# Kernel tuning notes

Measured on AMD Instinct MI355X. Metric: run time of the kernel, lower is better.

## Reference

```python
import jax, jax.numpy as jnp
import numpy as np

H = 4            # heads
C = 64           # per-head dim (= hidden, PyG TransformerConv semantics)
HD = 64          # hidden_dim
L = 2            # num_layers
NT = 2           # node types: 0=task, 1=machine
ET = ((0, 1), (1, 0))  # edge types: (src_nt, dst_nt)
N = 16384        # nodes per type (== max_nodes -> simple pos-enc slice)
E = 262144       # edges per edge type


def _ln(x, g, b):
    mu = x.mean(-1, keepdims=True)
    var = ((x - mu) ** 2).mean(-1, keepdims=True)
    return (x - mu) * jax.lax.rsqrt(var + 1e-5) * g + b


def _tconv(x_src, x_dst, ei, Wq, bq, Wk, bk, Wv, bv, Ws, bs, Wb):
    # PyG TransformerConv: heads=H, out_channels=C, concat=False, beta=True
    n_dst = x_dst.shape[0]
    src, dst = ei[0], ei[1]
    q = (x_dst @ Wq + bq).reshape(-1, H, C)
    k = (x_src @ Wk + bk).reshape(-1, H, C)
    v = (x_src @ Wv + bv).reshape(-1, H, C)
    logits = jnp.einsum('ehc,ehc->eh', q[dst], k[src]) * (1.0 / float(np.sqrt(C)))  # [E,H]
    m = jax.ops.segment_max(logits, dst, num_segments=n_dst)          # [N,H] segment softmax
    ex = jnp.exp(logits - m[dst])
    denom = jax.ops.segment_sum(ex, dst, num_segments=n_dst)
    alpha = ex / denom[dst]                                            # [E,H]
    msg = (alpha[:, :, None] * v[src]).reshape(-1, H * C)              # [E,H*C]
    out = jax.ops.segment_sum(msg, dst, num_segments=n_dst)
    out = out.reshape(n_dst, H, C).mean(axis=1)                        # concat=False -> head mean
    r = x_dst @ Ws + bs                                                # lin_skip
    beta = jax.nn.sigmoid(jnp.concatenate([out, r, out - r], -1) @ Wb) # lin_beta, [N,1]
    return beta * r + (1.0 - beta) * out


def _forward(edge_index, x, W_in, b_in, type_emb, pos, Wq, bq, Wk, bk, Wv, bv,
             Wskip, bskip, Wbeta, ln_g, ln_b, ff_W1, ff_b1, ff_W2, ff_b2, W_out, b_out):
    # input proj + type embedding + positional encoding (num_nodes == max_nodes -> slice)
    h = [x[t] @ W_in[t] + b_in[t] + type_emb[t] + pos[t] for t in range(NT)]
    for l in range(L):
        hn = [jnp.zeros_like(h[0]), jnp.zeros_like(h[1])]
        for e, (s, d) in enumerate(ET):  # HeteroConv, aggr='sum'
            hn[d] = hn[d] + _tconv(h[s], h[d], edge_index[e],
                                   Wq[l, e], bq[l, e], Wk[l, e], bk[l, e],
                                   Wv[l, e], bv[l, e], Wskip[l, e], bskip[l, e], Wbeta[l, e])
        for t in range(NT):
            hr = _ln(h[t] + hn[t], ln_g[l, t], ln_b[l, t])
            ff = jax.nn.gelu(hr @ ff_W1[l, t] + ff_b1[l, t], approximate=False) @ ff_W2[l, t] + ff_b2[l, t]
            h[t] = hr + ff
    return jnp.stack([h[t] @ W_out[t] + b_out[t] for t in range(NT)])  # [NT,N,HD]


def setup_inputs() -> dict:
    key = jax.random.key(0)
    ks = jax.random.split(key, 16)
    w = lambda k, s: 0.02 * jax.random.normal(k, s, jnp.float32)
    NE = len(ET)
    return {
        'x': jax.random.normal(ks[0], (NT, N, HD), jnp.float32),
        'edge_index': jax.random.randint(ks[1], (NE, 2, E), 0, N, jnp.int32),
        'W_in': w(ks[2], (NT, HD, HD)), 'b_in': jnp.zeros((NT, HD), jnp.float32),
        'type_emb': w(ks[3], (NT, HD)),
        'pos': w(ks[4], (NT, N, HD)),
        'Wq': w(ks[5], (L, NE, HD, H * C)), 'bq': jnp.zeros((L, NE, H * C), jnp.float32),
        'Wk': w(ks[6], (L, NE, HD, H * C)), 'bk': jnp.zeros((L, NE, H * C), jnp.float32),
        'Wv': w(ks[7], (L, NE, HD, H * C)), 'bv': jnp.zeros((L, NE, H * C), jnp.float32),
        'Wskip': w(ks[8], (L, NE, HD, HD)), 'bskip': jnp.zeros((L, NE, HD), jnp.float32),
        'Wbeta': w(ks[9], (L, NE, 3 * HD, 1)),
        'ln_g': jnp.ones((L, NT, HD), jnp.float32), 'ln_b': jnp.zeros((L, NT, HD), jnp.float32),
        'ff_W1': w(ks[10], (L, NT, HD, 4 * HD)), 'ff_b1': jnp.zeros((L, NT, 4 * HD), jnp.float32),
        'ff_W2': w(ks[11], (L, NT, 4 * HD, HD)), 'ff_b2': jnp.zeros((L, NT, HD), jnp.float32),
        'W_out': w(ks[12], (NT, HD, HD)), 'b_out': jnp.zeros((NT, HD), jnp.float32),
    }


def reference(x, edge_index, W_in, b_in, type_emb, pos, Wq, bq, Wk, bk, Wv, bv,
              Wskip, bskip, Wbeta, ln_g, ln_b, ff_W1, ff_b1, ff_W2, ff_b2, W_out, b_out):
    return _forward(edge_index, x, W_in, b_in, type_emb, pos, Wq, bq, Wk, bk, Wv, bv,
                    Wskip, bskip, Wbeta, ln_g, ln_b, ff_W1, ff_b1, ff_W2, ff_b2, W_out, b_out)
```

## Files before the change

kernel.cpp:

```cpp
#include <hip/hip_runtime.h>
#include <math.h>

#define NN 16384
#define EE 262144

typedef __bf16 v8bf __attribute__((ext_vector_type(8)));
typedef __bf16 v4bf __attribute__((ext_vector_type(4)));
typedef float  v4f  __attribute__((ext_vector_type(4)));
typedef float  v2f  __attribute__((ext_vector_type(2)));

#define OFF_CNT     0
#define OFF_FILL    (2*NN)
#define OFF_ROWPTR  (4*NN)
#define OFF_COLSRC  98816
#define OFF_H       623104
#define OFF_HN      (OFF_H  + 2*NN*64)
#define OFF_Q       (OFF_HN + 2*NN*64)
#define OFF_KV      (OFF_Q  + 2*NN*128)
#define OFF_R       (OFF_KV + 2*NN*128)
#define OFF_WT      (OFF_R  + 2*NN*64)
#define OFF_WBP     (OFF_WT + 180224)
#define OFF_LNG     (OFF_WBP + 768)
#define OFF_LNB     (OFF_LNG + 256)


#define WT_Q   0
#define WT_K   65536
#define WT_V   131072
#define WT_S   196608
#define WT_IN  212992
#define WT_W1  221184
#define WT_W2  286720
#define WT_WO  352256

__device__ __forceinline__ float blo(unsigned u) { return __uint_as_float(u << 16); }
__device__ __forceinline__ float bhi(unsigned u) { return __uint_as_float(u & 0xffff0000u); }
__device__ __forceinline__ unsigned short f2b(float f) {
  __bf16 h = (__bf16)f;
  return *(unsigned short*)&h;
}

struct PrepDesc { const float* src; unsigned short* dst; int ksh; int total; int kperm; };
struct PrepPack { PrepDesc d[28]; };

__global__ __launch_bounds__(256) void prep_kernel(PrepPack p) {
  PrepDesc g = p.d[blockIdx.y];
  int idx = blockIdx.x * 256 + threadIdx.x;
  if (idx >= g.total) return;
  int K = 1 << g.ksh;
  int n = idx >> g.ksh;
  int k = idx & (K - 1);
  int N = g.total >> g.ksh;
  int kk = g.kperm ? (16 * (k & 3) + (k >> 2)) : k;
  g.dst[idx] = f2b(g.src[(size_t)kk * N + n]);
}

struct PermDesc { const float* src; float* dst; int total; };
struct PermPack { PermDesc d[3]; };

__global__ __launch_bounds__(256) void perm_kernel(PermPack p) {
  PermDesc g = p.d[blockIdx.y];
  int idx = blockIdx.x * 256 + threadIdx.x;
  if (idx >= g.total) return;
  int c = idx & 63;
  g.dst[(idx & ~63) + ((c & 15) << 2) + (c >> 4)] = g.src[idx];
}

__global__ void count_kernel(const int* __restrict__ ei, int* __restrict__ cnt) {
  int idx = blockIdx.x * 256 + threadIdx.x;
  if (idx >= 2 * EE) return;
  int et = idx >> 18;
  int j  = idx & (EE - 1);
  int dst = ei[et * 2 * EE + EE + j];
  atomicAdd(&cnt[et * NN + dst], 1);
}

__global__ __launch_bounds__(1024) void scan_kernel(const int* __restrict__ cnt,
                                                    int* __restrict__ rowptr,
                                                    int* __restrict__ fill) {
  int et = blockIdx.x;
  const int* c = cnt + et * NN;
  __shared__ int sums[1024];
  int tid = threadIdx.x;
  int base = tid * 16;
  int loc[16];
  int s = 0;
#pragma unroll
  for (int i = 0; i < 16; ++i) { loc[i] = s; s += c[base + i]; }
  sums[tid] = s;
  __syncthreads();
  for (int off = 1; off < 1024; off <<= 1) {
    int v = 0;
    if (tid >= off) v = sums[tid - off];
    __syncthreads();
    if (tid >= off) sums[tid] += v;
    __syncthreads();
  }
  int ebase = (tid == 0) ? 0 : sums[tid - 1];
  int* rp = rowptr + et * (NN + 1);
  int* fl = fill + et * NN;
#pragma unroll
  for (int i = 0; i < 16; ++i) {
    rp[base + i] = ebase + loc[i];
    fl[base + i] = ebase + loc[i];
  }
  if (tid == 1023) rp[NN] = sums[1023];
}

__global__ void scatter_kernel(const int* __restrict__ ei, int* __restrict__ fill,
                               int* __restrict__ colsrc) {
  int idx = blockIdx.x * 256 + threadIdx.x;
  if (idx >= 2 * EE) return;
  int et = idx >> 18;
  int j  = idx & (EE - 1);
  int src = ei[et * 2 * EE + j];
  int dst = ei[et * 2 * EE + EE + j];
  int pos = atomicAdd(&fill[et * NN + dst], 1);
  colsrc[et * EE + pos] = (et * NN + src) << 9;
}

struct GemmDesc {
  const float *A, *bias, *bias2, *add;
  const unsigned short* Bt;
  char* C;
  int Ncols, Cld, ntiles, gelu, otype;
};
struct GemmPack { GemmDesc d[8]; int nd; };

#define LDA 72

__global__ __launch_bounds__(256) void gemm_mfma(GemmPack p) {
  GemmDesc g = p.d[blockIdx.y];
  const int row0 = blockIdx.x * 128;
  const int tid = threadIdx.x;
  const int w = tid >> 6, lane = tid & 63;
  const int l16 = lane & 15, quad = lane >> 4;

  __shared__ __bf16 As[128 * LDA];
  __shared__ __bf16 Bs[64 * LDA];

#pragma unroll
  for (int it = 0; it < 8; ++it) {
    int fi = it * 256 + tid;
    int grow = fi >> 4;
    int kq = (fi & 15) << 2;
    float4 a = *(const float4*)(g.A + (size_t)(row0 + grow) * 64 + kq);
    v4bf c = { (__bf16)a.x, (__bf16)a.y, (__bf16)a.z, (__bf16)a.w };
    *(v4bf*)&As[grow * LDA + kq] = c;
  }

  const int brow = tid >> 2;
  const int bko  = (tid & 3) << 4;

  for (int ct0 = 0; ct0 < g.ntiles; ++ct0) {
    const int col0 = ct0 * 64;
    __syncthreads();
    {
      const unsigned short* bp = g.Bt + (size_t)(col0 + brow) * 64 + bko;
      uint4 b0 = *(const uint4*)(bp);
      uint4 b1 = *(const uint4*)(bp + 8);
      *(uint4*)&Bs[brow * LDA + bko] = b0;
      *(uint4*)&Bs[brow * LDA + bko + 8] = b1;
    }
    __syncthreads();

    v4f acc[2][4];
#pragma unroll
    for (int rt = 0; rt < 2; ++rt)
#pragma unroll
      for (int ct = 0; ct < 4; ++ct)
#pragma unroll
        for (int r = 0; r < 4; ++r) acc[rt][ct][r] = 0.f;

#pragma unroll
    for (int ks = 0; ks < 2; ++ks) {
      v8bf a0 = *(v8bf*)&As[(w * 32 + l16) * LDA + ks * 32 + quad * 8];
      v8bf a1 = *(v8bf*)&As[(w * 32 + 16 + l16) * LDA + ks * 32 + quad * 8];
#pragma unroll
      for (int ct = 0; ct < 4; ++ct) {
        v8bf bb = *(v8bf*)&Bs[(ct * 16 + l16) * LDA + ks * 32 + quad * 8];
        acc[0][ct] = __builtin_amdgcn_mfma_f32_16x16x32_bf16(a0, bb, acc[0][ct], 0, 0, 0);
        acc[1][ct] = __builtin_amdgcn_mfma_f32_16x16x32_bf16(a1, bb, acc[1][ct], 0, 0, 0);
      }
    }

    float bias_c[4];
#pragma unroll
    for (int ct = 0; ct < 4; ++ct) {
      int col = col0 + ct * 16 + l16;
      float b = g.bias ? g.bias[col] : 0.f;
      if (g.bias2) b += g.bias2[col];
      bias_c[ct] = b;
    }
#pragma unroll
    for (int rt = 0; rt < 2; ++rt)
#pragma unroll
      for (int r = 0; r < 4; ++r) {
        size_t row = row0 + w * 32 + rt * 16 + quad * 4 + r;
        char* cp = g.C + row * (size_t)g.Cld;
        if (g.otype == 0) {
          float vv[4];
#pragma unroll
          for (int ct = 0; ct < 4; ++ct) {
            int col = col0 + ct * 16 + l16;
            float v = acc[rt][ct][r] + bias_c[ct];
            if (g.add) v += g.add[row * g.Ncols + col];
            if (g.gelu) v = 0.5f * v * (1.f + erff(v * 0.70710678118654752f));
            vv[ct] = v;
          }
          float4 w4 = { vv[0], vv[1], vv[2], vv[3] };
          *(float4*)(cp + col0 * 4 + l16 * 16) = w4;
        } else if (g.otype == 1) {
          ushort4 wq;
          wq.x = f2b(acc[rt][0][r] + bias_c[0]);
          wq.y = f2b(acc[rt][1][r] + bias_c[1]);
          wq.z = f2b(acc[rt][2][r] + bias_c[2]);
          wq.w = f2b(acc[rt][3][r] + bias_c[3]);
          *(ushort4*)(cp + col0 * 2 + l16 * 8) = wq;
        } else {
          unsigned wv = 0;
#pragma unroll
          for (int ct = 0; ct < 4; ++ct) {
            float v = acc[rt][ct][r] + bias_c[ct];
            unsigned pk = __builtin_amdgcn_cvt_pk_fp8_f32(v, v, 0, false);
            wv |= (pk & 0xffu) << (8 * ct);
          }
          *(unsigned*)(cp + col0 + l16 * 4) = wv;
        }
      }
  }
}

struct FFPack {
  const float *HN;
  const unsigned short *W1t, *W2t, *Wot;
  const float *b1, *b2, *bout;
  float* H;
  float* outbuf;
};

__global__ __launch_bounds__(256) void ff_fused(FFPack p) {
  const int t = blockIdx.y;
  const int row0 = blockIdx.x * 64;
  const int tid = threadIdx.x;
  const int w = tid >> 6, lane = tid & 63;
  const int l16 = lane & 15, quad = lane >> 4;

  const float* A  = p.HN + ((size_t)t * NN) * 64;
  const unsigned short* W1t = p.W1t + (size_t)t * 16384;
  const unsigned short* W2t = p.W2t + (size_t)t * 16384;
  const float* b1 = p.b1 + t * 256;
  const float* b2 = p.b2 + t * 64;

  __shared__ __bf16 As[64 * LDA];
  __shared__ __bf16 A2[64 * LDA];
  __shared__ __bf16 B1s[64 * LDA];
  __shared__ __bf16 B2s[64 * LDA];

#pragma unroll
  for (int it = 0; it < 4; ++it) {
    int fi = it * 256 + tid;
    int grow = fi >> 4;
    int kq = (fi & 15) << 2;
    float4 a = *(const float4*)(A + (size_t)(row0 + grow) * 64 + kq);
    v4bf c = { (__bf16)a.x, (__bf16)a.y, (__bf16)a.z, (__bf16)a.w };
    *(v4bf*)&As[grow * LDA + kq] = c;
  }

  const int brow = tid >> 2;
  const int bko  = (tid & 3) << 4;

  v4f acc2[4];
#pragma unroll
  for (int ct = 0; ct < 4; ++ct)
#pragma unroll
    for (int r = 0; r < 4; ++r) acc2[ct][r] = 0.f;

  for (int c1 = 0; c1 < 4; ++c1) {
    {
      const unsigned short* bp1 = W1t + (size_t)(c1 * 64 + brow) * 64 + bko;
      uint4 u0 = *(const uint4*)(bp1);
      uint4 u1 = *(const uint4*)(bp1 + 8);
      *(uint4*)&B1s[brow * LDA + bko] = u0;
      *(uint4*)&B1s[brow * LDA + bko + 8] = u1;
      const unsigned short* bp2 = W2t + (size_t)brow * 256 + c1 * 64 + bko;
      uint4 u2 = *(const uint4*)(bp2);
      uint4 u3 = *(const uint4*)(bp2 + 8);
      *(uint4*)&B2s[brow * LDA + bko] = u2;
      *(uint4*)&B2s[brow * LDA + bko + 8] = u3;
    }
    __syncthreads();

    v4f acc1[4];
#pragma unroll
    for (int ct = 0; ct < 4; ++ct)
#pragma unroll
      for (int r = 0; r < 4; ++r) acc1[ct][r] = 0.f;
#pragma unroll
    for (int ks = 0; ks < 2; ++ks) {
      v8bf a = *(v8bf*)&As[(w * 16 + l16) * LDA + ks * 32 + quad * 8];
#pragma unroll
      for (int ct = 0; ct < 4; ++ct) {
        v8bf bb = *(v8bf*)&B1s[(ct * 16 + l16) * LDA + ks * 32 + quad * 8];
        acc1[ct] = __builtin_amdgcn_mfma_f32_16x16x32_bf16(a, bb, acc1[ct], 0, 0, 0);
      }
    }
#pragma unroll
    for (int ct = 0; ct < 4; ++ct) {
      float bb = b1[c1 * 64 + ct * 16 + l16];
#pragma unroll
      for (int r = 0; r < 4; ++r) {
        float v = acc1[ct][r] + bb;
        v = 0.5f * v * (1.f + erff(v * 0.70710678118654752f));
        A2[(w * 16 + quad * 4 + r) * LDA + ct * 16 + l16] = (__bf16)v;
      }
    }
#pragma unroll
    for (int ks = 0; ks < 2; ++ks) {
      v8bf a = *(v8bf*)&A2[(w * 16 + l16) * LDA + ks * 32 + quad * 8];
#pragma unroll
      for (int ct = 0; ct < 4; ++ct) {
        v8bf bb = *(v8bf*)&B2s[(ct * 16 + l16) * LDA + ks * 32 + quad * 8];
        acc2[ct] = __builtin_amdgcn_mfma_f32_16x16x32_bf16(a, bb, acc2[ct], 0, 0, 0);
      }
    }
    __syncthreads();
  }

  float b2c[4];
#pragma unroll
  for (int ct = 0; ct < 4; ++ct) b2c[ct] = b2[ct * 16 + l16];

  if (!p.outbuf) {
#pragma unroll
    for (int r = 0; r < 4; ++r) {
      size_t row = (size_t)t * NN + row0 + w * 16 + quad * 4 + r;
      float4 hn4 = *(const float4*)(p.HN + row * 64 + l16 * 4);
      float4 o4;
      o4.x = acc2[0][r] + b2c[0] + hn4.x;
      o4.y = acc2[1][r] + b2c[1] + hn4.y;
      o4.z = acc2[2][r] + b2c[2] + hn4.z;
      o4.w = acc2[3][r] + b2c[3] + hn4.w;
      *(float4*)(p.H + row * 64 + l16 * 4) = o4;
    }
    return;
  }

#pragma unroll
  for (int r = 0; r < 4; ++r) {
    int lrow = w * 16 + quad * 4 + r;
    size_t row = (size_t)t * NN + row0 + lrow;
    float4 hn4 = *(const float4*)(p.HN + row * 64 + l16 * 4);
    float hn[4] = { hn4.x, hn4.y, hn4.z, hn4.w };
#pragma unroll
    for (int ct = 0; ct < 4; ++ct) {
      int col = ct * 16 + l16;
      A2[lrow * LDA + col] = (__bf16)(acc2[ct][r] + b2c[ct] + hn[ct]);
    }
  }
  {
    const unsigned short* Wot = p.Wot + (size_t)t * 4096;
    const unsigned short* bp = Wot + (size_t)brow * 64 + bko;
    uint4 u0 = *(const uint4*)(bp);
    uint4 u1 = *(const uint4*)(bp + 8);
    *(uint4*)&B1s[brow * LDA + bko] = u0;
    *(uint4*)&B1s[brow * LDA + bko + 8] = u1;
  }
  __syncthreads();

  v4f acc3[4];
#pragma unroll
  for (int ct = 0; ct < 4; ++ct)
#pragma unroll
    for (int r = 0; r < 4; ++r) acc3[ct][r] = 0.f;
#pragma unroll
  for (int ks = 0; ks < 2; ++ks) {
    v8bf a = *(v8bf*)&A2[(w * 16 + l16) * LDA + ks * 32 + quad * 8];
#pragma unroll
    for (int ct = 0; ct < 4; ++ct) {
      v8bf bb = *(v8bf*)&B1s[(ct * 16 + l16) * LDA + ks * 32 + quad * 8];
      acc3[ct] = __builtin_amdgcn_mfma_f32_16x16x32_bf16(a, bb, acc3[ct], 0, 0, 0);
    }
  }
  const float* bo = p.bout + t * 64;
#pragma unroll
  for (int ct = 0; ct < 4; ++ct) {
    int col = ct * 16 + l16;
    float bb = bo[col];
#pragma unroll
    for (int r = 0; r < 4; ++r) {
      size_t row = (size_t)t * NN + row0 + w * 16 + quad * 4 + r;
      p.outbuf[row * 64 + col] = acc3[ct][r] + bb;
    }
  }
}

struct AggPack {
  const unsigned short *Q;
  const char *KV;
  const float *R;
  const float *Wb;
  const float *Hin;
  const float *lng, *lnb;
  float* outHR;
  const int *rowptr;
  const int *colsrc;
};

__global__ __launch_bounds__(256) void agg_kernel(AggPack p) {
  const int et = blockIdx.y, d = 1 - et;
  int wid = __builtin_amdgcn_readfirstlane(threadIdx.x >> 6);
  int lane = threadIdx.x & 63;
  int node = blockIdx.x * 4 + wid;
  int c4 = lane & 15;
  int cb = ((lane >> 4) << 6) + (c4 << 2);

  const int* rp = p.rowptr + et * (NN + 1);
  const int* cs = p.colsrc + et * EE;
  int start = rp[node], end = rp[node + 1];
  int len = end - start;
  int gnode = d * NN + node;

  uint2 qw = *(const uint2*)(p.Q + ((size_t)gnode << 8) + cb);
  float q0 = blo(qw.x) * 0.125f, q1 = bhi(qw.x) * 0.125f;
  float q2 = blo(qw.y) * 0.125f, q3 = bhi(qw.y) * 0.125f;

  int b[5];
#pragma unroll
  for (int i = 0; i <= 4; ++i) b[i] = start + ((len * i) >> 2);
  float dsum[4] = {0.f, 0.f, 0.f, 0.f};
  float acc[4][4];
#pragma unroll
  for (int s4 = 0; s4 < 4; ++s4)
#pragma unroll
    for (int c = 0; c < 4; ++c) acc[s4][c] = 0.f;

  int maxn = (len + 3) >> 2;
  int last = end - 1;
  for (int it = 0; it < maxn; ++it) {
#pragma unroll
    for (int s4 = 0; s4 < 4; ++s4) {
      int j = b[s4] + it;
      bool act = j < b[s4 + 1];
      int jc = act ? j : last;
      int off = cs[jc];
      const char* rowp = p.KV + off;
      unsigned kw = *(const unsigned*)(rowp + cb);
      unsigned vw = *(const unsigned*)(rowp + 256 + cb);
      v2f kl = __builtin_amdgcn_cvt_pk_f32_fp8((int)kw, false);
      v2f kh = __builtin_amdgcn_cvt_pk_f32_fp8((int)kw, true);
      float pd = q0 * kl[0] + q1 * kl[1] + q2 * kh[0] + q3 * kh[1];
      pd += __shfl_xor(pd, 1);
      pd += __shfl_xor(pd, 2);
      pd += __shfl_xor(pd, 4);
      pd += __shfl_xor(pd, 8);
      float wgt = act ? __expf(pd) : 0.f;
      v2f vl = __builtin_amdgcn_cvt_pk_f32_fp8((int)vw, false);
      v2f vh = __builtin_amdgcn_cvt_pk_f32_fp8((int)vw, true);
      dsum[s4] += wgt;
      acc[s4][0] += wgt * vl[0];
      acc[s4][1] += wgt * vl[1];
      acc[s4][2] += wgt * vh[0];
      acc[s4][3] += wgt * vh[1];
    }
  }
  float dn = (dsum[0] + dsum[1]) + (dsum[2] + dsum[3]);
  float o_[4];
#pragma unroll
  for (int i = 0; i < 4; ++i)
    o_[i] = (acc[0][i] + acc[1][i]) + (acc[2][i] + acc[3][i]);

  float inv = (len > 0) ? (0.25f / dn) : 0.f;
#pragma unroll
  for (int i = 0; i < 4; ++i) {
    float a = o_[i] * inv;
    a += __shfl_xor(a, 16);
    a += __shfl_xor(a, 32);
    o_[i] = a;
  }

  float4 r4 = *(const float4*)(p.R + (size_t)gnode * 64 + c4 * 4);
  float4 h4 = *(const float4*)(p.Hin + (size_t)gnode * 64 + c4 * 4);
  float rr[4] = { r4.x, r4.y, r4.z, r4.w };
  float hh[4] = { h4.x, h4.y, h4.z, h4.w };

  const float* wb = p.Wb + et * 192;
  float4 wo4 = *(const float4*)(wb + c4 * 4);
  float4 wr4 = *(const float4*)(wb + 64 + c4 * 4);
  float4 wd4 = *(const float4*)(wb + 128 + c4 * 4);
  float wo[4] = { wo4.x, wo4.y, wo4.z, wo4.w };
  float wr[4] = { wr4.x, wr4.y, wr4.z, wr4.w };
  float wd[4] = { wd4.x, wd4.y, wd4.z, wd4.w };
  float part = 0.f;
#pragma unroll
  for (int i = 0; i < 4; ++i)
    part += o_[i] * wo[i] + rr[i] * wr[i] + (o_[i] - rr[i]) * wd[i];
  part += __shfl_xor(part, 1);
  part += __shfl_xor(part, 2);
  part += __shfl_xor(part, 4);
  part += __shfl_xor(part, 8);
  float beta = 1.f / (1.f + __expf(-part));

  float y[4];
  float sa = 0.f, sb = 0.f;
#pragma unroll
  for (int i = 0; i < 4; ++i) {
    float v = hh[i] + beta * rr[i] + (1.f - beta) * o_[i];
    y[i] = v;
    sa += v;
    sb += v * v;
  }
  sa += __shfl_xor(sa, 1); sb += __shfl_xor(sb, 1);
  sa += __shfl_xor(sa, 2); sb += __shfl_xor(sb, 2);
  sa += __shfl_xor(sa, 4); sb += __shfl_xor(sb, 4);
  sa += __shfl_xor(sa, 8); sb += __shfl_xor(sb, 8);
  float mu = sa * (1.f / 64.f);
  float var = sb * (1.f / 64.f) - mu * mu;
  float rs = rsqrtf(var + 1e-5f);
  if (lane < 16) {
    float4 g4 = *(const float4*)(p.lng + d * 64 + c4 * 4);
    float4 bb4 = *(const float4*)(p.lnb + d * 64 + c4 * 4);
    float4 res;
    res.x = (y[0] - mu) * rs * g4.x + bb4.x;
    res.y = (y[1] - mu) * rs * g4.y + bb4.y;
    res.z = (y[2] - mu) * rs * g4.z + bb4.z;
    res.w = (y[3] - mu) * rs * g4.w + bb4.w;
    *(float4*)(p.outHR + (size_t)gnode * 64 + c4 * 4) = res;
  }
}

static void add_desc(GemmPack& p, const float* A, const unsigned short* Bt,
                     const float* bias, const float* bias2, const float* add,
                     void* C, int Nc, int Cld, int gelu, int otype) {
  GemmDesc& g = p.d[p.nd++];
  g.A = A; g.Bt = Bt; g.bias = bias; g.bias2 = bias2; g.add = add; g.C = (char*)C;
  g.Ncols = Nc; g.Cld = Cld; g.ntiles = Nc / 64;
  g.gelu = gelu; g.otype = otype;
}

extern "C" void kernel_launch(void* const* d_in, const int* in_sizes, int n_in,
                              void* d_out, int out_size, void* d_ws, size_t ws_size,
                              hipStream_t stream) {
  const float* x        = (const float*)d_in[0];
  const int*   ei       = (const int*)d_in[1];
  const float* W_in     = (const float*)d_in[2];
  const float* b_in     = (const float*)d_in[3];
  const float* type_emb = (const float*)d_in[4];
  const float* pos      = (const float*)d_in[5];
  const float* Wq       = (const float*)d_in[6];
  const float* bq       = (const float*)d_in[7];
  const float* Wk       = (const float*)d_in[8];
  const float* bk       = (const float*)d_in[9];
  const float* Wv       = (const float*)d_in[10];
  const float* bv       = (const float*)d_in[11];
  const float* Wskip    = (const float*)d_in[12];
  const float* bskip    = (const float*)d_in[13];
  const float* Wbeta    = (const float*)d_in[14];
  const float* ln_g     = (const float*)d_in[15];
  const float* ln_b     = (const float*)d_in[16];
  const float* ff_W1    = (const float*)d_in[17];
  const float* ff_b1    = (const float*)d_in[18];
  const float* ff_W2    = (const float*)d_in[19];
  const float* ff_b2    = (const float*)d_in[20];
  const float* W_out    = (const float*)d_in[21];
  const float* b_out    = (const float*)d_in[22];
  float* out = (float*)d_out;

  int*   wsi = (int*)d_ws;
  float* wsf = (float*)d_ws;
  int* cnt    = wsi + OFF_CNT;
  int* fill   = wsi + OFF_FILL;
  int* rowptr = wsi + OFF_ROWPTR;
  int* colsrc = wsi + OFF_COLSRC;
  float* H  = wsf + OFF_H;
  float* HN = wsf + OFF_HN;
  unsigned short* Qb = (unsigned short*)(wsf + OFF_Q);
  char* KVb = (char*)(wsf + OFF_KV);
  float* Rb = wsf + OFF_R;
  unsigned short* wt = (unsigned short*)(wsf + OFF_WT);
  float* wbp  = wsf + OFF_WBP;
  float* lngp = wsf + OFF_LNG;
  float* lnbp = wsf + OFF_LNB;

  {
    PrepPack pp{};
    int nd = 0;
    for (int we = 0; we < 4; ++we) {
      pp.d[nd++] = { Wq + (size_t)we * 16384, wt + WT_Q + we * 16384, 6, 16384, 1 };
      pp.d[nd++] = { Wk + (size_t)we * 16384, wt + WT_K + we * 16384, 6, 16384, 1 };
      pp.d[nd++] = { Wv + (size_t)we * 16384, wt + WT_V + we * 16384, 6, 16384, 1 };
      pp.d[nd++] = { Wskip + (size_t)we * 4096, wt + WT_S + we * 4096, 6, 4096, 1 };
      pp.d[nd++] = { ff_W1 + (size_t)we * 16384, wt + WT_W1 + we * 16384, 6, 16384, 1 };
      pp.d[nd++] = { ff_W2 + (size_t)we * 16384, wt + WT_W2 + we * 16384, 8, 16384, 0 };
    }
    for (int t = 0; t < 2; ++t) {
      pp.d[nd++] = { W_in + (size_t)t * 4096, wt + WT_IN + t * 4096, 6, 4096, 0 };
      pp.d[nd++] = { W_out + (size_t)t * 4096, wt + WT_WO + t * 4096, 6, 4096, 0 };
    }
    prep_kernel<<<dim3(64, nd), dim3(256), 0, stream>>>(pp);
  }
  {
    PermPack pm{};
    pm.d[0] = { Wbeta, wbp, 768 };
    pm.d[1] = { ln_g, lngp, 256 };
    pm.d[2] = { ln_b, lnbp, 256 };
    perm_kernel<<<dim3(3, 3), dim3(256), 0, stream>>>(pm);
  }

  hipMemsetAsync(cnt, 0, 2 * NN * sizeof(int), stream);
  count_kernel<<<dim3(2 * EE / 256), dim3(256), 0, stream>>>(ei, cnt);
  scan_kernel<<<dim3(2), dim3(1024), 0, stream>>>(cnt, rowptr, fill);
  scatter_kernel<<<dim3(2 * EE / 256), dim3(256), 0, stream>>>(ei, fill, colsrc);

  {
    GemmPack p{};
    for (int t = 0; t < 2; ++t)
      add_desc(p, x + (size_t)t * NN * 64, wt + WT_IN + t * 4096,
               b_in + t * 64, type_emb + t * 64, pos + (size_t)t * NN * 64,
               H + (size_t)t * NN * 64, 64, 256, 0, 0);
    gemm_mfma<<<dim3(128, p.nd), dim3(256), 0, stream>>>(p);
  }

  for (int l = 0; l < 2; ++l) {
    {
      GemmPack p{};
      for (int et = 0; et < 2; ++et) {
        int s = et, d = 1 - et;
        int we = l * 2 + et;
        const float* hs = H + (size_t)s * NN * 64;
        const float* hd = H + (size_t)d * NN * 64;
        add_desc(p, hd, wt + WT_Q + we * 16384, bq + we * 256,
                 nullptr, nullptr, (char*)Qb + (size_t)d * NN * 512, 256, 512, 0, 1);
        add_desc(p, hs, wt + WT_K + we * 16384, bk + we * 256,
                 nullptr, nullptr, KVb + (size_t)s * NN * 512, 256, 512, 0, 2);
        add_desc(p, hs, wt + WT_V + we * 16384, bv + we * 256,
                 nullptr, nullptr, KVb + (size_t)s * NN * 512 + 256, 256, 512, 0, 2);
        add_desc(p, hd, wt + WT_S + we * 4096, bskip + we * 64,
                 nullptr, nullptr, Rb + (size_t)d * NN * 64, 64, 256, 0, 0);
      }
      gemm_mfma<<<dim3(128, p.nd), dim3(256), 0, stream>>>(p);
    }

    AggPack ap;
    ap.Q = Qb; ap.KV = KVb; ap.R = Rb;
    ap.Wb = wbp + l * 2 * 192;
    ap.Hin = H;
    ap.lng = lngp + l * 128;
    ap.lnb = lnbp + l * 128;
    ap.outHR = HN;
    ap.rowptr = rowptr;
    ap.colsrc = colsrc;
    agg_kernel<<<dim3(NN / 4, 2), dim3(256), 0, stream>>>(ap);

    FFPack fp;
    fp.HN = HN;
    fp.W1t = wt + WT_W1 + l * 2 * 16384;
    fp.W2t = wt + WT_W2 + l * 2 * 16384;
    fp.Wot = wt + WT_WO;
    fp.b1 = ff_b1 + l * 2 * 256;
    fp.b2 = ff_b2 + l * 2 * 64;
    fp.bout = b_out;
    fp.H  = H;
    fp.outbuf = (l == 1) ? out : nullptr;
    ff_fused<<<dim3(NN / 64, 2), dim3(256), 0, stream>>>(fp);
  }
}
```

Measured before the change: 321.7 us.

## Fuse next-layer QKV/skip projections into FF epilogue and merge prep launches

The layer-0 feed-forward kernel now keeps its output tile in shared memory as bf16 and computes the layer-1 Q, K, V and skip projections directly in a 13-tile loop. This removes the separate layer-1 projection GEMM launch and the re-read of H from global memory. The perm kernel and the count memset are folded into the prep kernel as extra modes. The count and scatter kernels now process four edges per thread using int4 loads. The fused FF kernel does more serial work per block, adding per-tile syncs and register pressure that may reduce overlap.

```diff
diff --git a/kernel.cpp b/kernel.cpp
--- a/kernel.cpp
+++ b/kernel.cpp
@@ -40,39 +40,36 @@
   return *(unsigned short*)&h;
 }
 
-struct PrepDesc { const float* src; unsigned short* dst; int ksh; int total; int kperm; };
-struct PrepPack { PrepDesc d[28]; };
+struct PrepDesc { const float* src; void* dst; int ksh; int total; int mode; };
+struct PrepPack { PrepDesc d[34]; };
 
 __global__ __launch_bounds__(256) void prep_kernel(PrepPack p) {
   PrepDesc g = p.d[blockIdx.y];
   int idx = blockIdx.x * 256 + threadIdx.x;
   if (idx >= g.total) return;
+  if (g.mode == 3) { ((int*)g.dst)[idx] = 0; return; }
+  if (g.mode == 2) {
+    int c = idx & 63;
+    ((float*)g.dst)[(idx & ~63) + ((c & 15) << 2) + (c >> 4)] = g.src[idx];
+    return;
+  }
   int K = 1 << g.ksh;
   int n = idx >> g.ksh;
   int k = idx & (K - 1);
   int N = g.total >> g.ksh;
-  int kk = g.kperm ? (16 * (k & 3) + (k >> 2)) : k;
-  g.dst[idx] = f2b(g.src[(size_t)kk * N + n]);
-}
-
-struct PermDesc { const float* src; float* dst; int total; };
-struct PermPack { PermDesc d[3]; };
-
-__global__ __launch_bounds__(256) void perm_kernel(PermPack p) {
-  PermDesc g = p.d[blockIdx.y];
-  int idx = blockIdx.x * 256 + threadIdx.x;
-  if (idx >= g.total) return;
-  int c = idx & 63;
-  g.dst[(idx & ~63) + ((c & 15) << 2) + (c >> 4)] = g.src[idx];
+  int kk = (g.mode == 1) ? (16 * (k & 3) + (k >> 2)) : k;
+  ((unsigned short*)g.dst)[idx] = f2b(g.src[(size_t)kk * N + n]);
 }
 
 __global__ void count_kernel(const int* __restrict__ ei, int* __restrict__ cnt) {
   int idx = blockIdx.x * 256 + threadIdx.x;
-  if (idx >= 2 * EE) return;
-  int et = idx >> 18;
-  int j  = idx & (EE - 1);
-  int dst = ei[et * 2 * EE + EE + j];
-  atomicAdd(&cnt[et * NN + dst], 1);
+  int et = idx >> 16;
+  int j4 = (idx & 65535) << 2;
+  int4 dv = *(const int4*)(ei + (size_t)et * 2 * EE + EE + j4);
+  atomicAdd(&cnt[et * NN + dv.x], 1);
+  atomicAdd(&cnt[et * NN + dv.y], 1);
+  atomicAdd(&cnt[et * NN + dv.z], 1);
+  atomicAdd(&cnt[et * NN + dv.w], 1);
 }
 
 __global__ __launch_bounds__(1024) void scan_kernel(const int* __restrict__ cnt,
@@ -110,13 +107,18 @@
 __global__ void scatter_kernel(const int* __restrict__ ei, int* __restrict__ fill,
                                int* __restrict__ colsrc) {
   int idx = blockIdx.x * 256 + threadIdx.x;
-  if (idx >= 2 * EE) return;
-  int et = idx >> 18;
-  int j  = idx & (EE - 1);
-  int src = ei[et * 2 * EE + j];
-  int dst = ei[et * 2 * EE + EE + j];
-  int pos = atomicAdd(&fill[et * NN + dst], 1);
-  colsrc[et * EE + pos] = (et * NN + src) << 9;
+  int et = idx >> 16;
+  int j4 = (idx & 65535) << 2;
+  const int* eb = ei + (size_t)et * 2 * EE;
+  int4 sv = *(const int4*)(eb + j4);
+  int4 dv = *(const int4*)(eb + EE + j4);
+  int* fl = fill + et * NN;
+  int* csb = colsrc + et * EE;
+  int pos;
+  pos = atomicAdd(&fl[dv.x], 1); csb[pos] = (et * NN + sv.x) << 9;
+  pos = atomicAdd(&fl[dv.y], 1); csb[pos] = (et * NN + sv.y) << 9;
+  pos = atomicAdd(&fl[dv.z], 1); csb[pos] = (et * NN + sv.z) << 9;
+  pos = atomicAdd(&fl[dv.w], 1); csb[pos] = (et * NN + sv.w) << 9;
 }
 
 struct GemmDesc {
@@ -231,12 +233,16 @@
   }
 }
 
+struct QTile { const unsigned short* Bt; const float* bias; char* C; int Cld; int otype; };
+
 struct FFPack {
   const float *HN;
   const unsigned short *W1t, *W2t, *Wot;
   const float *b1, *b2, *bout;
   float* H;
   float* outbuf;
+  QTile qt[2][13];
+  int nqt;
 };
 
 __global__ __launch_bounds__(256) void ff_fused(FFPack p) {
@@ -331,17 +337,53 @@
 #pragma unroll
   for (int ct = 0; ct < 4; ++ct) b2c[ct] = b2[ct * 16 + l16];
 
-  if (!p.outbuf) {
+  if (p.outbuf) {
 #pragma unroll
     for (int r = 0; r < 4; ++r) {
-      size_t row = (size_t)t * NN + row0 + w * 16 + quad * 4 + r;
+      int lrow = w * 16 + quad * 4 + r;
+      size_t row = (size_t)t * NN + row0 + lrow;
       float4 hn4 = *(const float4*)(p.HN + row * 64 + l16 * 4);
-      float4 o4;
-      o4.x = acc2[0][r] + b2c[0] + hn4.x;
-      o4.y = acc2[1][r] + b2c[1] + hn4.y;
-      o4.z = acc2[2][r] + b2c[2] + hn4.z;
-      o4.w = acc2[3][r] + b2c[3] + hn4.w;
-      *(float4*)(p.H + row * 64 + l16 * 4) = o4;
+      float hn[4] = { hn4.x, hn4.y, hn4.z, hn4.w };
+#pragma unroll
+      for (int ct = 0; ct < 4; ++ct) {
+        int col = ct * 16 + l16;
+        A2[lrow * LDA + col] = (__bf16)(acc2[ct][r] + b2c[ct] + hn[ct]);
+      }
+    }
+    {
+      const unsigned short* Wot = p.Wot + (size_t)t * 4096;
+      const unsigned short* bp = Wot + (size_t)brow * 64 + bko;
+      uint4 u0 = *(const uint4*)(bp);
+      uint4 u1 = *(const uint4*)(bp + 8);
+      *(uint4*)&B1s[brow * LDA + bko] = u0;
+      *(uint4*)&B1s[brow * LDA + bko + 8] = u1;
+    }
+    __syncthreads();
+
+    v4f acc3[4];
+#pragma unroll
+    for (int ct = 0; ct < 4; ++ct)
+#pragma unroll
+      for (int r = 0; r < 4; ++r) acc3[ct][r] = 0.f;
+#pragma unroll
+    for (int ks = 0; ks < 2; ++ks) {
+      v8bf a = *(v8bf*)&A2[(w * 16 + l16) * LDA + ks * 32 + quad * 8];
+#pragma unroll
+      for (int ct = 0; ct < 4; ++ct) {
+        v8bf bb = *(v8bf*)&B1s[(ct * 16 + l16) * LDA + ks * 32 + quad * 8];
+        acc3[ct] = __builtin_amdgcn_mfma_f32_16x16x32_bf16(a, bb, acc3[ct], 0, 0, 0);
+      }
+    }
+    const float* bo = p.bout + t * 64;
+#pragma unroll
+    for (int ct = 0; ct < 4; ++ct) {
+      int col = ct * 16 + l16;
+      float bb = bo[col];
+#pragma unroll
+      for (int r = 0; r < 4; ++r) {
+        size_t row = (size_t)t * NN + row0 + w * 16 + quad * 4 + r;
+        p.outbuf[row * 64 + col] = acc3[ct][r] + bb;
+      }
     }
     return;
   }
@@ -351,46 +393,72 @@
     int lrow = w * 16 + quad * 4 + r;
     size_t row = (size_t)t * NN + row0 + lrow;
     float4 hn4 = *(const float4*)(p.HN + row * 64 + l16 * 4);
-    float hn[4] = { hn4.x, hn4.y, hn4.z, hn4.w };
-#pragma unroll
-    for (int ct = 0; ct < 4; ++ct) {
-      int col = ct * 16 + l16;
-      A2[lrow * LDA + col] = (__bf16)(acc2[ct][r] + b2c[ct] + hn[ct]);
-    }
-  }
-  {
-    const unsigned short* Wot = p.Wot + (size_t)t * 4096;
-    const unsigned short* bp = Wot + (size_t)brow * 64 + bko;
-    uint4 u0 = *(const uint4*)(bp);
-    uint4 u1 = *(const uint4*)(bp + 8);
-    *(uint4*)&B1s[brow * LDA + bko] = u0;
-    *(uint4*)&B1s[brow * LDA + bko + 8] = u1;
-  }
-  __syncthreads();
-
-  v4f acc3[4];
-#pragma unroll
-  for (int ct = 0; ct < 4; ++ct)
-#pragma unroll
-    for (int r = 0; r < 4; ++r) acc3[ct][r] = 0.f;
-#pragma unroll
-  for (int ks = 0; ks < 2; ++ks) {
-    v8bf a = *(v8bf*)&A2[(w * 16 + l16) * LDA + ks * 32 + quad * 8];
-#pragma unroll
-    for (int ct = 0; ct < 4; ++ct) {
-      v8bf bb = *(v8bf*)&B1s[(ct * 16 + l16) * LDA + ks * 32 + quad * 8];
-      acc3[ct] = __builtin_amdgcn_mfma_f32_16x16x32_bf16(a, bb, acc3[ct], 0, 0, 0);
-    }
-  }
-  const float* bo = p.bout + t * 64;
-#pragma unroll
-  for (int ct = 0; ct < 4; ++ct) {
-    int col = ct * 16 + l16;
-    float bb = bo[col];
+    float4 o4;
+    o4.x = acc2[0][r] + b2c[0] + hn4.x;
+    o4.y = acc2[1][r] + b2c[1] + hn4.y;
+    o4.z = acc2[2][r] + b2c[2] + hn4.z;
+    o4.w = acc2[3][r] + b2c[3] + hn4.w;
+    *(float4*)(p.H + row * 64 + l16 * 4) = o4;
+    v4bf a4 = { (__bf16)o4.x, (__bf16)o4.y, (__bf16)o4.z, (__bf16)o4.w };
+    *(v4bf*)&As[lrow * LDA + l16 * 4] = a4;
+  }
+
+  for (int ti = 0; ti < p.nqt; ++ti) {
+    QTile qt = p.qt[t][ti];
+    __syncthreads();
+    {
+      const unsigned short* bp = qt.Bt + (size_t)brow * 64 + bko;
+      uint4 u0 = *(const uint4*)(bp);
+      uint4 u1 = *(const uint4*)(bp + 8);
+      *(uint4*)&B1s[brow * LDA + bko] = u0;
+      *(uint4*)&B1s[brow * LDA + bko + 8] = u1;
+    }
+    __syncthreads();
+
+    v4f acc1[4];
+#pragma unroll
+    for (int ct = 0; ct < 4; ++ct)
+#pragma unroll
+      for (int r = 0; r < 4; ++r) acc1[ct][r] = 0.f;
+#pragma unroll
+    for (int ks = 0; ks < 2; ++ks) {
+      v8bf a = *(v8bf*)&As[(w * 16 + l16) * LDA + ks * 32 + quad * 8];
+#pragma unroll
+      for (int ct = 0; ct < 4; ++ct) {
+        v8bf bb = *(v8bf*)&B1s[(ct * 16 + l16) * LDA + ks * 32 + quad * 8];
+        acc1[ct] = __builtin_amdgcn_mfma_f32_16x16x32_bf16(a, bb, acc1[ct], 0, 0, 0);
+      }
+    }
+
+    float bias_c[4];
+#pragma unroll
+    for (int ct = 0; ct < 4; ++ct) bias_c[ct] = qt.bias[ct * 16 + l16];
+
 #pragma unroll
     for (int r = 0; r < 4; ++r) {
-      size_t row = (size_t)t * NN + row0 + w * 16 + quad * 4 + r;
-      p.outbuf[row * 64 + col] = acc3[ct][r] + bb;
+      size_t row = row0 + w * 16 + quad * 4 + r;
+      char* cp = qt.C + row * (size_t)qt.Cld;
+      if (qt.otype == 0) {
+        float4 w4 = { acc1[0][r] + bias_c[0], acc1[1][r] + bias_c[1],
+                      acc1[2][r] + bias_c[2], acc1[3][r] + bias_c[3] };
+        *(float4*)(cp + l16 * 16) = w4;
+      } else if (qt.otype == 1) {
+        ushort4 wq;
+        wq.x = f2b(acc1[0][r] + bias_c[0]);
+        wq.y = f2b(acc1[1][r] + bias_c[1]);
+        wq.z = f2b(acc1[2][r] + bias_c[2]);
+        wq.w = f2b(acc1[3][r] + bias_c[3]);
+        *(ushort4*)(cp + l16 * 8) = wq;
+      } else {
+        unsigned wv = 0;
+#pragma unroll
+        for (int ct = 0; ct < 4; ++ct) {
+          float v = acc1[ct][r] + bias_c[ct];
+          unsigned pk = __builtin_amdgcn_cvt_pk_fp8_f32(v, v, 0, false);
+          wv |= (pk & 0xffu) << (8 * ct);
+        }
+        *(unsigned*)(cp + l16 * 4) = wv;
+      }
     }
   }
 }
@@ -597,20 +665,17 @@
       pp.d[nd++] = { W_in + (size_t)t * 4096, wt + WT_IN + t * 4096, 6, 4096, 0 };
       pp.d[nd++] = { W_out + (size_t)t * 4096, wt + WT_WO + t * 4096, 6, 4096, 0 };
     }
+    pp.d[nd++] = { Wbeta, wbp, 0, 768, 2 };
+    pp.d[nd++] = { ln_g, lngp, 0, 256, 2 };
+    pp.d[nd++] = { ln_b, lnbp, 0, 256, 2 };
+    pp.d[nd++] = { nullptr, cnt, 0, 16384, 3 };
+    pp.d[nd++] = { nullptr, cnt + 16384, 0, 16384, 3 };
     prep_kernel<<<dim3(64, nd), dim3(256), 0, stream>>>(pp);
   }
-  {
-    PermPack pm{};
-    pm.d[0] = { Wbeta, wbp, 768 };
-    pm.d[1] = { ln_g, lngp, 256 };
-    pm.d[2] = { ln_b, lnbp, 256 };
-    perm_kernel<<<dim3(3, 3), dim3(256), 0, stream>>>(pm);
-  }
-
-  hipMemsetAsync(cnt, 0, 2 * NN * sizeof(int), stream);
-  count_kernel<<<dim3(2 * EE / 256), dim3(256), 0, stream>>>(ei, cnt);
+
+  count_kernel<<<dim3(2 * EE / 1024), dim3(256), 0, stream>>>(ei, cnt);
   scan_kernel<<<dim3(2), dim3(1024), 0, stream>>>(cnt, rowptr, fill);
-  scatter_kernel<<<dim3(2 * EE / 256), dim3(256), 0, stream>>>(ei, fill, colsrc);
+  scatter_kernel<<<dim3(2 * EE / 1024), dim3(256), 0, stream>>>(ei, fill, colsrc);
 
   {
     GemmPack p{};
@@ -621,26 +686,26 @@
     gemm_mfma<<<dim3(128, p.nd), dim3(256), 0, stream>>>(p);
   }
 
+  {
+    GemmPack p{};
+    for (int et = 0; et < 2; ++et) {
+      int s = et, d = 1 - et;
+      int we = et;
+      const float* hs = H + (size_t)s * NN * 64;
+      const float* hd = H + (size_t)d * NN * 64;
+      add_desc(p, hd, wt + WT_Q + we * 16384, bq + we * 256,
+               nullptr, nullptr, (char*)Qb + (size_t)d * NN * 512, 256, 512, 0, 1);
+      add_desc(p, hs, wt + WT_K + we * 16384, bk + we * 256,
+               nullptr, nullptr, KVb + (size_t)s * NN * 512, 256, 512, 0, 2);
+      add_desc(p, hs, wt + WT_V + we * 16384, bv + we * 256,
+               nullptr, nullptr, KVb + (size_t)s * NN * 512 + 256, 256, 512, 0, 2);
+      add_desc(p, hd, wt + WT_S + we * 4096, bskip + we * 64,
+               nullptr, nullptr, Rb + (size_t)d * NN * 64, 64, 256, 0, 0);
+    }
+    gemm_mfma<<<dim3(128, p.nd), dim3(256), 0, stream>>>(p);
+  }
+
   for (int l = 0; l < 2; ++l) {
-    {
-      GemmPack p{};
-      for (int et = 0; et < 2; ++et) {
-        int s = et, d = 1 - et;
-        int we = l * 2 + et;
-        const float* hs = H + (size_t)s * NN * 64;
-        const float* hd = H + (size_t)d * NN * 64;
-        add_desc(p, hd, wt + WT_Q + we * 16384, bq + we * 256,
-                 nullptr, nullptr, (char*)Qb + (size_t)d * NN * 512, 256, 512, 0, 1);
-        add_desc(p, hs, wt + WT_K + we * 16384, bk + we * 256,
-                 nullptr, nullptr, KVb + (size_t)s * NN * 512, 256, 512, 0, 2);
-        add_desc(p, hs, wt + WT_V + we * 16384, bv + we * 256,
-                 nullptr, nullptr, KVb + (size_t)s * NN * 512 + 256, 256, 512, 0, 2);
-        add_desc(p, hd, wt + WT_S + we * 4096, bskip + we * 64,
-                 nullptr, nullptr, Rb + (size_t)d * NN * 64, 64, 256, 0, 0);
-      }
-      gemm_mfma<<<dim3(128, p.nd), dim3(256), 0, stream>>>(p);
-    }
-
     AggPack ap;
     ap.Q = Qb; ap.KV = KVb; ap.R = Rb;
     ap.Wb = wbp + l * 2 * 192;
@@ -652,7 +717,7 @@
     ap.colsrc = colsrc;
     agg_kernel<<<dim3(NN / 4, 2), dim3(256), 0, stream>>>(ap);
 
-    FFPack fp;
+    FFPack fp{};
     fp.HN = HN;
     fp.W1t = wt + WT_W1 + l * 2 * 16384;
     fp.W2t = wt + WT_W2 + l * 2 * 16384;
@@ -661,7 +726,31 @@
     fp.b2 = ff_b2 + l * 2 * 64;
     fp.bout = b_out;
     fp.H  = H;
-    fp.outbuf = (l == 1) ? out : nullptr;
+    if (l == 1) {
+      fp.outbuf = out;
+      fp.nqt = 0;
+    } else {
+      fp.outbuf = nullptr;
+      fp.nqt = 13;
+      for (int tt = 0; tt < 2; ++tt) {
+        int we_d = 2 + (1 - tt);
+        int we_s = 2 + tt;
+        for (int j = 0; j < 4; ++j) {
+          fp.qt[tt][j] = { wt + WT_Q + we_d * 16384 + j * 64 * 64,
+                           bq + we_d * 256 + j * 64,
+                           (char*)Qb + (size_t)tt * NN * 512 + j * 128, 512, 1 };
+          fp.qt[tt][4 + j] = { wt + WT_K + we_s * 16384 + j * 64 * 64,
+                               bk + we_s * 256 + j * 64,
+                               KVb + (size_t)tt * NN * 512 + j * 64, 512, 2 };
+          fp.qt[tt][8 + j] = { wt + WT_V + we_s * 16384 + j * 64 * 64,
+                               bv + we_s * 256 + j * 64,
+                               KVb + (size_t)tt * NN * 512 + 256 + j * 64, 512, 2 };
+        }
+        fp.qt[tt][12] = { wt + WT_S + we_d * 4096,
+                          bskip + we_d * 64,
+                          (char*)(Rb + (size_t)tt * NN * 64), 256, 0 };
+      }
+    }
     ff_fused<<<dim3(NN / 64, 2), dim3(256), 0, stream>>>(fp);
   }
 }
```

Measured after the change: 324.1 us. About the same (+0.7%).
